# Kernel tuning notes

Measured on AMD Instinct MI355X. Metric: run time of the kernel, lower is better.

## Reference

```python
import jax, jax.numpy as jnp
import numpy as np

N_NODES = 100000
N_EDGES = 800000
HIDDEN = 256
BOTTLENECK = 32


def setup_inputs() -> dict:
    key = jax.random.key(0)
    k1, k2, k3, k4 = jax.random.split(key, 4)
    x = jax.random.normal(k1, (N_NODES, HIDDEN), dtype=jnp.float32)
    edge_index = jax.random.randint(k2, (2, N_EDGES), 0, N_NODES, dtype=jnp.int64)
    # PyG GCNConv linear weights, init per module: normal(std=1e-5), zero bias
    W_down = jax.random.normal(k3, (BOTTLENECK, HIDDEN), dtype=jnp.float32) * 1e-5
    b_down = jnp.zeros((BOTTLENECK,), dtype=jnp.float32)
    W_up = jax.random.normal(k4, (HIDDEN, BOTTLENECK), dtype=jnp.float32) * 1e-5
    b_up = jnp.zeros((HIDDEN,), dtype=jnp.float32)
    return {"x": x, "edge_index": edge_index, "W_down": W_down, "b_down": b_down,
            "W_up": W_up, "b_up": b_up}


def reference(x, edge_index, W_down, b_down, W_up, b_up):
    N = x.shape[0]
    loops = jnp.arange(N, dtype=edge_index.dtype)
    # gcn_norm with self-loops (edge weight = 1), symmetric normalization
    row = jnp.concatenate([edge_index[0], loops])  # source nodes
    col = jnp.concatenate([edge_index[1], loops])  # target nodes
    deg = jax.ops.segment_sum(jnp.ones(row.shape[0], dtype=x.dtype), col, num_segments=N)
    dinv = jnp.where(deg > 0, jax.lax.rsqrt(deg), 0.0)
    norm = dinv[row] * dinv[col]  # [E+N]

    def gcn_conv(h, W, b):
        h = h @ W.T                                   # [N, out]
        msgs = h[row] * norm[:, None]                 # gather + weight
        return jax.ops.segment_sum(msgs, col, num_segments=N) + b

    h = jax.nn.relu(gcn_conv(x, W_down, b_down))      # down-proj conv + act
    out = gcn_conv(h, W_up, b_up) + x                 # up-proj conv + skip
    return out
```

## Files before the change

### kernel.cpp

```cpp
#include <hip/hip_runtime.h>
#include <hip/hip_bf16.h>
#include <stdint.h>

#define HID 256
#define BOT 32

typedef short short8 __attribute__((ext_vector_type(8)));
typedef unsigned short ushort8 __attribute__((ext_vector_type(8)));
typedef float floatx4 __attribute__((ext_vector_type(4)));

__device__ __forceinline__ unsigned short f2bu(float f) {
    return (unsigned short)(__float_as_uint(f) >> 16);
}
__device__ __forceinline__ float bu2f(unsigned short u) {
    return __uint_as_float((unsigned int)u << 16);
}
__device__ __forceinline__ short8 pack8(float4 a, float4 b) {
    short8 r;
    r[0] = (short)f2bu(a.x); r[1] = (short)f2bu(a.y);
    r[2] = (short)f2bu(a.z); r[3] = (short)f2bu(a.w);
    r[4] = (short)f2bu(b.x); r[5] = (short)f2bu(b.y);
    r[6] = (short)f2bu(b.z); r[7] = (short)f2bu(b.w);
    return r;
}


__global__ void k_detect(const int* __restrict__ ei, int* __restrict__ flags) {
    int t = threadIdx.x;
    int found = 0;
    for (int i = 0; i < 8; ++i) {
        int slot = 2 * (t * 8 + i) + 1;
        if (ei[slot] != 0) found = 1;
    }
    unsigned long long b = __ballot(found);
    if (t == 0) flags[0] = (b == 0ULL) ? 1 : 0;
}

__global__ void k_deg(const int* __restrict__ ei, int E, int* __restrict__ deg,
                      const int* __restrict__ flags) {
    int mode = flags[0];
    int e = blockIdx.x * blockDim.x + threadIdx.x;
    if (e >= E) return;
    int d = mode ? ei[2 * E + 2 * e] : ei[E + e];
    atomicAdd(deg + d, 1);
}

__global__ void k_dinv(const int* __restrict__ deg, float* __restrict__ dinv, int N) {
    int i = blockIdx.x * blockDim.x + threadIdx.x;
    if (i < N) dinv[i] = rsqrtf((float)(deg[i] + 1));
}

__global__ __launch_bounds__(256) void k_alloc(const int* __restrict__ deg,
                                               int* __restrict__ start,
                                               int* __restrict__ cur,
                                               int* __restrict__ cursor, int N) {
    __shared__ int sdata[256];
    __shared__ int sbase;
    int tid = threadIdx.x;
    int i = blockIdx.x * 256 + tid;
    int d = (i < N) ? deg[i] : 0;
    sdata[tid] = d;
    __syncthreads();
    for (int off = 1; off < 256; off <<= 1) {
        int t = (tid >= off) ? sdata[tid - off] : 0;
        __syncthreads();
        sdata[tid] += t;
        __syncthreads();
    }
    if (tid == 0) sbase = atomicAdd(cursor, sdata[255]);
    __syncthreads();
    if (i < N) {
        int st = sbase + sdata[tid] - d;
        start[i] = st;
        cur[i] = st;
    }
}

__global__ void k_fill(const int* __restrict__ ei, int E,
                       const float* __restrict__ dinv,
                       int* __restrict__ cur, int2* __restrict__ srcw,
                       const int* __restrict__ flags) {
    int mode = flags[0];
    int e = blockIdx.x * blockDim.x + threadIdx.x;
    if (e >= E) return;
    int s, d;
    if (mode) { s = ei[2 * e]; d = ei[2 * E + 2 * e]; }
    else      { s = ei[e];     d = ei[E + e]; }
    float w = dinv[s] * dinv[d];
    int slot = atomicAdd(cur + d, 1);
    srcw[slot] = make_int2(s, __float_as_int(w));
}

__global__ __launch_bounds__(256) void k_gemm_down(
    const float* __restrict__ x, const float* __restrict__ Wd,
    unsigned short* __restrict__ P, int N, int nwaves)
{
    int wid  = (blockIdx.x * 256 + threadIdx.x) >> 6;
    int lane = threadIdx.x & 63;
    int m = lane & 15, q = lane >> 4;

    short8 bfr[2][8];
    #pragma unroll
    for (int jt = 0; jt < 2; ++jt) {
        const float4* wr = (const float4*)(Wd + (size_t)(jt * 16 + m) * HID);
        #pragma unroll
        for (int ks = 0; ks < 8; ++ks) {
            int c = (ks * 32 + q * 8) >> 2;
            bfr[jt][ks] = pack8(wr[c], wr[c + 1]);
        }
    }

    int tiles = (N + 15) >> 4;
    for (int t = wid; t < tiles; t += nwaves) {
        int n0 = t << 4;
        int row = n0 + m; if (row >= N) row = N - 1;
        const float4* xr = (const float4*)(x + (size_t)row * HID);
        floatx4 acc0 = {0.f, 0.f, 0.f, 0.f};
        floatx4 acc1 = {0.f, 0.f, 0.f, 0.f};
        #pragma unroll
        for (int ks = 0; ks < 8; ++ks) {
            int c = (ks * 32 + q * 8) >> 2;
            short8 af = pack8(xr[c], xr[c + 1]);
            acc0 = __builtin_amdgcn_mfma_f32_16x16x32_bf16(bfr[0][ks], af, acc0, 0, 0, 0);
            acc1 = __builtin_amdgcn_mfma_f32_16x16x32_bf16(bfr[1][ks], af, acc1, 0, 0, 0);
        }
        if (n0 + m < N) {
            unsigned int* pr = (unsigned int*)(P + (size_t)(n0 + m) * BOT);
            uint2 v0, v1;
            v0.x = (unsigned int)f2bu(acc0[0]) | ((unsigned int)f2bu(acc0[1]) << 16);
            v0.y = (unsigned int)f2bu(acc0[2]) | ((unsigned int)f2bu(acc0[3]) << 16);
            v1.x = (unsigned int)f2bu(acc1[0]) | ((unsigned int)f2bu(acc1[1]) << 16);
            v1.y = (unsigned int)f2bu(acc1[2]) | ((unsigned int)f2bu(acc1[3]) << 16);
            *(uint2*)(pr + q * 2)     = v0;
            *(uint2*)(pr + 8 + q * 2) = v1;
        }
    }
}

__global__ __launch_bounds__(256) void k_gather(
    const unsigned short* __restrict__ feat, const float* __restrict__ dinv,
    const int* __restrict__ start, const int* __restrict__ endp,
    const int2* __restrict__ srcw, const float* __restrict__ bias,
    unsigned short* __restrict__ dst, int N, int relu_bias)
{
    int t = blockIdx.x * 256 + threadIdx.x;
    int n = t >> 2, jq = (t & 3) * 8;
    if (n >= N) return;
    float di = dinv[n];
    float w0 = di * di;
    float acc[8];
    ushort8 sv = *(const ushort8*)(feat + (size_t)n * BOT + jq);
    #pragma unroll
    for (int i = 0; i < 8; ++i) acc[i] = w0 * bu2f(sv[i]);
    int k = start[n], en = endp[n];
    for (; k + 1 < en; k += 2) {
        int2 p0 = srcw[k];
        int2 p1 = srcw[k + 1];
        ushort8 f0 = *(const ushort8*)(feat + (size_t)p0.x * BOT + jq);
        ushort8 f1 = *(const ushort8*)(feat + (size_t)p1.x * BOT + jq);
        float wa = __int_as_float(p0.y), wb = __int_as_float(p1.y);
        #pragma unroll
        for (int i = 0; i < 8; ++i) acc[i] += wa * bu2f(f0[i]);
        #pragma unroll
        for (int i = 0; i < 8; ++i) acc[i] += wb * bu2f(f1[i]);
    }
    if (k < en) {
        int2 p = srcw[k];
        ushort8 f0 = *(const ushort8*)(feat + (size_t)p.x * BOT + jq);
        float wa = __int_as_float(p.y);
        #pragma unroll
        for (int i = 0; i < 8; ++i) acc[i] += wa * bu2f(f0[i]);
    }
    if (relu_bias) {
        #pragma unroll
        for (int i = 0; i < 8; ++i) {
            float a = acc[i] + bias[jq + i];
            acc[i] = a > 0.f ? a : 0.f;
        }
    }
    ushort8 o;
    #pragma unroll
    for (int i = 0; i < 8; ++i) o[i] = f2bu(acc[i]);
    *(ushort8*)(dst + (size_t)n * BOT + jq) = o;
}

__global__ __launch_bounds__(256) void k_out(
    const unsigned short* __restrict__ A2, const float* __restrict__ x,
    const float* __restrict__ Wup, const float* __restrict__ bup,
    float* __restrict__ out, int N, int nwaves)
{
    int wid  = (blockIdx.x * 256 + threadIdx.x) >> 6;
    int lane = threadIdx.x & 63;
    int m = lane & 15, q = lane >> 4;

    short8 bfr[16];
    #pragma unroll
    for (int ft = 0; ft < 16; ++ft) {
        const float4* wr = (const float4*)(Wup + (size_t)(ft * 16 + m) * BOT);
        bfr[ft] = pack8(wr[q * 2], wr[q * 2 + 1]);
    }

    int tiles = (N + 15) >> 4;
    for (int t = wid; t < tiles; t += nwaves) {
        int n0 = t << 4;
        int arow = n0 + m; if (arow >= N) arow = N - 1;
        short8 af = *(const short8*)(A2 + (size_t)arow * BOT + q * 8);
        const float4* xrow = (const float4*)(x + (size_t)arow * HID);
        floatx4* orow = (floatx4*)(out + (size_t)arow * HID);
        bool ok = (n0 + m) < N;
        #pragma unroll
        for (int ft = 0; ft < 16; ++ft) {
            floatx4 acc = {0.f, 0.f, 0.f, 0.f};
            acc = __builtin_amdgcn_mfma_f32_16x16x32_bf16(bfr[ft], af, acc, 0, 0, 0);
            if (ok) {
                int c = ft * 4 + q;
                float4 xv = xrow[c];
                float4 bb = *(const float4*)(bup + ft * 16 + q * 4);
                floatx4 res;
                res[0] = acc[0] + bb.x + xv.x;
                res[1] = acc[1] + bb.y + xv.y;
                res[2] = acc[2] + bb.z + xv.z;
                res[3] = acc[3] + bb.w + xv.w;
                __builtin_nontemporal_store(res, &orow[c]);
            }
        }
    }
}

extern "C" void kernel_launch(void* const* d_in, const int* in_sizes, int n_in,
                              void* d_out, int out_size, void* d_ws, size_t ws_size,
                              hipStream_t stream) {
    const float* x  = (const float*)d_in[0];
    const int*   ei = (const int*)d_in[1];
    const float* Wd = (const float*)d_in[2];
    const float* bd = (const float*)d_in[3];
    const float* Wu = (const float*)d_in[4];
    const float* bu = (const float*)d_in[5];
    float* out = (float*)d_out;

    int N = in_sizes[0] / HID;
    int E = in_sizes[1] / 2;

    char* ws = (char*)d_ws;
    int*   flags = (int*)ws;
    int*   deg   = (int*)(ws + 16);
    float* dinv  = (float*)(ws + 16 + (size_t)N * 4);
    int*   startp= (int*)(ws + 16 + (size_t)N * 8);
    int*   curp  = (int*)(ws + 16 + (size_t)N * 12);
    int2*  srcw  = (int2*)(ws + 16 + (size_t)N * 16);
    unsigned short* P  = (unsigned short*)(ws + 16 + (size_t)N * 16 + (size_t)E * 8);
    unsigned short* A1 = (unsigned short*)(ws + 16 + (size_t)N * 16 + (size_t)E * 8 + (size_t)N * 64);

    (void)hipMemsetAsync(ws, 0, 16 + (size_t)N * 4, stream);
    k_detect<<<1, 64, 0, stream>>>(ei, flags);
    k_deg<<<(E + 255) / 256, 256, 0, stream>>>(ei, E, deg, flags);
    k_dinv<<<(N + 255) / 256, 256, 0, stream>>>(deg, dinv, N);

    k_alloc<<<(N + 255) / 256, 256, 0, stream>>>(deg, startp, curp, flags + 1, N);
    k_fill<<<(E + 255) / 256, 256, 0, stream>>>(ei, E, dinv, curp, srcw, flags);

    int gblocks = 782;
    k_gemm_down<<<gblocks, 256, 0, stream>>>(x, Wd, P, N, gblocks * 4);
    int gthreads = N * 4;
    k_gather<<<(gthreads + 255) / 256, 256, 0, stream>>>(P, dinv, startp, curp, srcw, bd, A1, N, 1);

    k_gather<<<(gthreads + 255) / 256, 256, 0, stream>>>(A1, dinv, startp, curp, srcw, bd, P, N, 0);

    int oblocks = 782;
    k_out<<<oblocks, 256, 0, stream>>>(P, x, Wu, bu, out, N, oblocks * 4);
}
```

Before: 375.1 us.

## Fuse dinv into alloc, shuffle-share edge loads in gather, split out GEMM per wave

The dinv computation moves into the prefix-sum alloc kernel, which removes one launch. In the gather kernel, the four threads that share a node each load one edge record and broadcast it with width-4 shuffles, so each thread no longer loads every edge record itself. The output kernel gives each wave one tile and half of the feature columns instead of a grid-stride loop with all 16 weight fragments kept in registers, which trades register pressure and reuse for more parallelism. The down-GEMM grid is now sized from the tile count rather than fixed at 782 blocks.

```diff
diff --git a/kernel.cpp b/kernel.cpp
--- a/kernel.cpp
+++ b/kernel.cpp
@@ -45,12 +45,8 @@
     atomicAdd(deg + d, 1);
 }
 
-__global__ void k_dinv(const int* __restrict__ deg, float* __restrict__ dinv, int N) {
-    int i = blockIdx.x * blockDim.x + threadIdx.x;
-    if (i < N) dinv[i] = rsqrtf((float)(deg[i] + 1));
-}
-
 __global__ __launch_bounds__(256) void k_alloc(const int* __restrict__ deg,
+                                               float* __restrict__ dinv,
                                                int* __restrict__ start,
                                                int* __restrict__ cur,
                                                int* __restrict__ cursor, int N) {
@@ -59,6 +55,7 @@
     int tid = threadIdx.x;
     int i = blockIdx.x * 256 + tid;
     int d = (i < N) ? deg[i] : 0;
+    if (i < N) dinv[i] = rsqrtf((float)(d + 1));
     sdata[tid] = d;
     __syncthreads();
     for (int off = 1; off < 256; off <<= 1) {
@@ -144,7 +141,7 @@
     unsigned short* __restrict__ dst, int N, int relu_bias)
 {
     int t = blockIdx.x * 256 + threadIdx.x;
-    int n = t >> 2, jq = (t & 3) * 8;
+    int n = t >> 2, tg = t & 3, jq = tg * 8;
     if (n >= N) return;
     float di = dinv[n];
     float w0 = di * di;
@@ -153,23 +150,18 @@
     #pragma unroll
     for (int i = 0; i < 8; ++i) acc[i] = w0 * bu2f(sv[i]);
     int k = start[n], en = endp[n];
-    for (; k + 1 < en; k += 2) {
-        int2 p0 = srcw[k];
-        int2 p1 = srcw[k + 1];
-        ushort8 f0 = *(const ushort8*)(feat + (size_t)p0.x * BOT + jq);
-        ushort8 f1 = *(const ushort8*)(feat + (size_t)p1.x * BOT + jq);
-        float wa = __int_as_float(p0.y), wb = __int_as_float(p1.y);
-        #pragma unroll
-        for (int i = 0; i < 8; ++i) acc[i] += wa * bu2f(f0[i]);
-        #pragma unroll
-        for (int i = 0; i < 8; ++i) acc[i] += wb * bu2f(f1[i]);
-    }
-    if (k < en) {
-        int2 p = srcw[k];
-        ushort8 f0 = *(const ushort8*)(feat + (size_t)p.x * BOT + jq);
-        float wa = __int_as_float(p.y);
-        #pragma unroll
-        for (int i = 0; i < 8; ++i) acc[i] += wa * bu2f(f0[i]);
+    for (; k < en; k += 4) {
+        int kk = k + tg;
+        int2 p = make_int2(0, 0);
+        if (kk < en) p = srcw[kk];
+        #pragma unroll
+        for (int e = 0; e < 4; ++e) {
+            int   src = __shfl(p.x, e, 4);
+            float w   = __uint_as_float((unsigned int)__shfl(p.y, e, 4));
+            ushort8 f = *(const ushort8*)(feat + (size_t)src * BOT + jq);
+            #pragma unroll
+            for (int i = 0; i < 8; ++i) acc[i] += w * bu2f(f[i]);
+        }
     }
     if (relu_bias) {
         #pragma unroll
@@ -187,42 +179,38 @@
 __global__ __launch_bounds__(256) void k_out(
     const unsigned short* __restrict__ A2, const float* __restrict__ x,
     const float* __restrict__ Wup, const float* __restrict__ bup,
-    float* __restrict__ out, int N, int nwaves)
+    float* __restrict__ out, int N)
 {
-    int wid  = (blockIdx.x * 256 + threadIdx.x) >> 6;
+    int gw   = (blockIdx.x * 256 + threadIdx.x) >> 6;
     int lane = threadIdx.x & 63;
     int m = lane & 15, q = lane >> 4;
-
-    short8 bfr[16];
-    #pragma unroll
-    for (int ft = 0; ft < 16; ++ft) {
+    int tiles = (N + 15) >> 4;
+    int t = gw >> 1, h = gw & 1;
+    if (t >= tiles) return;
+
+    int n0 = t << 4;
+    int arow = n0 + m; if (arow >= N) arow = N - 1;
+    short8 af = *(const short8*)(A2 + (size_t)arow * BOT + q * 8);
+    const float4* xrow = (const float4*)(x + (size_t)arow * HID);
+    floatx4* orow = (floatx4*)(out + (size_t)arow * HID);
+    bool ok = (n0 + m) < N;
+    #pragma unroll
+    for (int i = 0; i < 8; ++i) {
+        int ft = h * 8 + i;
         const float4* wr = (const float4*)(Wup + (size_t)(ft * 16 + m) * BOT);
-        bfr[ft] = pack8(wr[q * 2], wr[q * 2 + 1]);
-    }
-
-    int tiles = (N + 15) >> 4;
-    for (int t = wid; t < tiles; t += nwaves) {
-        int n0 = t << 4;
-        int arow = n0 + m; if (arow >= N) arow = N - 1;
-        short8 af = *(const short8*)(A2 + (size_t)arow * BOT + q * 8);
-        const float4* xrow = (const float4*)(x + (size_t)arow * HID);
-        floatx4* orow = (floatx4*)(out + (size_t)arow * HID);
-        bool ok = (n0 + m) < N;
-        #pragma unroll
-        for (int ft = 0; ft < 16; ++ft) {
-            floatx4 acc = {0.f, 0.f, 0.f, 0.f};
-            acc = __builtin_amdgcn_mfma_f32_16x16x32_bf16(bfr[ft], af, acc, 0, 0, 0);
-            if (ok) {
-                int c = ft * 4 + q;
-                float4 xv = xrow[c];
-                float4 bb = *(const float4*)(bup + ft * 16 + q * 4);
-                floatx4 res;
-                res[0] = acc[0] + bb.x + xv.x;
-                res[1] = acc[1] + bb.y + xv.y;
-                res[2] = acc[2] + bb.z + xv.z;
-                res[3] = acc[3] + bb.w + xv.w;
-                __builtin_nontemporal_store(res, &orow[c]);
-            }
+        short8 bfr = pack8(wr[q * 2], wr[q * 2 + 1]);
+        floatx4 acc = {0.f, 0.f, 0.f, 0.f};
+        acc = __builtin_amdgcn_mfma_f32_16x16x32_bf16(bfr, af, acc, 0, 0, 0);
+        if (ok) {
+            int c = ft * 4 + q;
+            float4 xv = xrow[c];
+            float4 bb = *(const float4*)(bup + ft * 16 + q * 4);
+            floatx4 res;
+            res[0] = acc[0] + bb.x + xv.x;
+            res[1] = acc[1] + bb.y + xv.y;
+            res[2] = acc[2] + bb.z + xv.z;
+            res[3] = acc[3] + bb.w + xv.w;
+            __builtin_nontemporal_store(res, &orow[c]);
         }
     }
 }
@@ -254,18 +242,18 @@
     (void)hipMemsetAsync(ws, 0, 16 + (size_t)N * 4, stream);
     k_detect<<<1, 64, 0, stream>>>(ei, flags);
     k_deg<<<(E + 255) / 256, 256, 0, stream>>>(ei, E, deg, flags);
-    k_dinv<<<(N + 255) / 256, 256, 0, stream>>>(deg, dinv, N);
-
-    k_alloc<<<(N + 255) / 256, 256, 0, stream>>>(deg, startp, curp, flags + 1, N);
+
+    k_alloc<<<(N + 255) / 256, 256, 0, stream>>>(deg, dinv, startp, curp, flags + 1, N);
     k_fill<<<(E + 255) / 256, 256, 0, stream>>>(ei, E, dinv, curp, srcw, flags);
 
-    int gblocks = 782;
+    int tiles = (N + 15) / 16;
+    int gblocks = (tiles + 3) / 4;
     k_gemm_down<<<gblocks, 256, 0, stream>>>(x, Wd, P, N, gblocks * 4);
     int gthreads = N * 4;
     k_gather<<<(gthreads + 255) / 256, 256, 0, stream>>>(P, dinv, startp, curp, srcw, bd, A1, N, 1);
 
     k_gather<<<(gthreads + 255) / 256, 256, 0, stream>>>(A1, dinv, startp, curp, srcw, bd, P, N, 0);
 
-    int oblocks = 782;
-    k_out<<<oblocks, 256, 0, stream>>>(P, x, Wu, bu, out, N, oblocks * 4);
-}
+    int oblocks = (tiles * 2 + 3) / 4;
+    k_out<<<oblocks, 256, 0, stream>>>(P, x, Wu, bu, out, N);
+}
```

After: 360.1 us. 4.0% less time.
